# Kernel tuning notes

Hardware: AMD Instinct MI355X
Metric: run time of the kernel (lower is better)

The kernel has to match this reference:

```python
import jax, jax.numpy as jnp
import numpy as np

K = 15  # knn neighbors (init kwarg k)


def setup_inputs() -> dict:
    key = jax.random.key(0)
    ks = jax.random.split(key, 6)
    N, E, IN, H = 4096, 24576, 3, 64
    x = jax.random.normal(ks[0], (N, IN), jnp.float32)
    edges = jax.random.randint(ks[1], (2, E), 0, N, jnp.int32)
    # torch Linear weights: shape [out, in], y = x @ W.T
    Wt = jax.random.normal(ks[2], (H, IN), jnp.float32) * 0.1   # DevConv W_theta
    Wp = jax.random.normal(ks[3], (H, H), jnp.float32) * 0.1    # DevConv W_phi
    Wq = jax.random.normal(ks[4], (H, H), jnp.float32) * 0.1    # W_q
    Wk = jax.random.normal(ks[5], (H, H), jnp.float32) * 0.1    # W_k
    return {"x": x, "edges": edges, "Wt": Wt, "Wp": Wp, "Wq": Wq, "Wk": Wk}


def _knn_edges(x, k):
    # pairwise squared distances via gram trick; exclude self (loop=False)
    N = x.shape[0]
    sq = jnp.sum(x * x, axis=-1)
    d = sq[:, None] + sq[None, :] - 2.0 * (x @ x.T)  # [N, N]
    d = d.at[jnp.arange(N), jnp.arange(N)].set(jnp.inf)
    _, nbr = jax.lax.top_k(-d, k)  # [N, k] nearest neighbor indices
    row = jnp.repeat(jnp.arange(N, dtype=jnp.int32), k)
    col = nbr.reshape(-1).astype(jnp.int32)
    return row, col  # flow='target_to_source': row = center node


def reference(x, edges, Wt, Wp, Wq, Wk):
    N = x.shape[0]
    # ---- knn graph + edge union (dedup is a no-op for max aggregation) ----
    kr, kc = _knn_edges(x, K)
    row_e = jnp.concatenate([edges[0], kr])
    col_e = jnp.concatenate([edges[1], kc])
    # ---- DevConv: f_i = W_phi ( max_{j in N(i)} W_theta (x_j - x_i) ) ----
    diff = x[col_e] - x[row_e]                 # [Etot, IN]
    msg = diff @ Wt.T                          # [Etot, H]
    agg = jax.ops.segment_max(msg, row_e, num_segments=N)
    agg = jnp.where(jnp.isfinite(agg), agg, 0.0)
    feat = agg @ Wp.T                          # [N, H]
    # ---- scatter-softmax attention over original edges ----
    r, c = edges[0], edges[1]
    q = feat @ Wq.T
    k = feat @ Wk.T
    att = jnp.sum(q[r] * k[c], axis=-1)        # [E]
    m = jax.ops.segment_max(att, r, num_segments=N)
    ex = jnp.exp(att - m[r])
    den = jax.ops.segment_sum(ex, r, num_segments=N)
    attn = ex / den[r]
    # ---- estimated adjacency A_s = S @ A @ S^T (dense canonical form) ----
    S = jnp.zeros((N, N), x.dtype).at[r, c].add(attn)   # coalesce = sum dups
    A = jnp.zeros((N, N), x.dtype).at[r, c].add(1.0)
    return (S @ A) @ S.T
```

## Files before the change

kernel.cpp:

```cpp
#include <hip/hip_runtime.h>
#include <math.h>

#define N_NODES 4096
#define H 64
#define NE 24576
#define KNN 15
#define KBUF 448
#define MAXP_ROW 512
#define BSLOT 32

typedef float vfloat4 __attribute__((ext_vector_type(4)));

__device__ __forceinline__ int mbcnt64(unsigned long long m) {
    int lo = __builtin_amdgcn_mbcnt_lo((unsigned int)m, 0u);
    return __builtin_amdgcn_mbcnt_hi((unsigned int)(m >> 32), lo);
}

__global__ __launch_bounds__(256) void k_init(int* __restrict__ cursR, int* __restrict__ cursC,
                                              const float* __restrict__ x, float4* __restrict__ xp,
                                              const float* __restrict__ Wp, const float* __restrict__ Wq,
                                              const float* __restrict__ Wk,
                                              float* __restrict__ WpT, float* __restrict__ WqT,
                                              float* __restrict__ WkT) {
    int tid = blockIdx.x * 256 + threadIdx.x;
    if (tid < N_NODES) {
        cursR[tid] = 0; cursC[tid] = 0;
        float a = x[tid * 3], b = x[tid * 3 + 1], c = x[tid * 3 + 2];
        xp[tid] = make_float4(a, b, c, a * a + b * b + c * c);
    }
    if (tid < H * H) {
        int k = tid >> 6, h = tid & 63;
        WpT[k * H + h] = Wp[h * H + k];
        WqT[k * H + h] = Wq[h * H + k];
        WkT[k * H + h] = Wk[h * H + k];
    }
}

__global__ __launch_bounds__(64) void k_knn(const float4* __restrict__ xp, int* __restrict__ knn_idx,
                                            const int* __restrict__ edges, int* __restrict__ cursR,
                                            int* __restrict__ cursC, int* __restrict__ colRb,
                                            int* __restrict__ c2cb, float2* __restrict__ jav) {
    __shared__ unsigned long long cb[KBUF];
    const int lane = threadIdx.x;
    const int i = blockIdx.x;

    if (i < NE / 64) {
        int e = i * 64 + lane;
        int r = edges[e], c = edges[NE + e];
        int p = atomicAdd(&cursR[r], 1);
        int q = atomicAdd(&cursC[c], 1);
        if (p < BSLOT && q < BSLOT) {
            colRb[r * BSLOT + p] = c;
            c2cb[r * BSLOT + p] = c * BSLOT + q;
            ((int*)jav)[2 * (c * BSLOT + q)] = r;
        }
    }

    const float4 pi = xp[i];
    unsigned long long tauKey;
    int cnt;

    auto sort64 = [&](unsigned long long key) -> unsigned long long {
#pragma unroll
        for (int k = 2; k <= 64; k <<= 1) {
#pragma unroll
            for (int j = 32; j > 0; j >>= 1) {
                if (j >= k) continue;
                unsigned long long other = __shfl_xor(key, j);
                bool asc = ((lane & k) == 0);
                bool takeMin = (((lane & j) == 0) == asc);
                bool less = key < other;
                key = (takeMin == less) ? key : other;
            }
        }
        return key;
    };

    auto tighten = [&]() {
        __builtin_amdgcn_wave_barrier();
        int n = (cnt + 63) >> 6;
        unsigned long long v[7];
        unsigned long long kmin = ~0ull;
#pragma unroll
        for (int t = 0; t < 7; ++t) {
            v[t] = ~0ull;
            if (t < n) {
                int s = t * 64 + lane;
                if (s < cnt) v[t] = cb[s];
                kmin = (v[t] < kmin) ? v[t] : kmin;
            }
        }
        unsigned long long T = __shfl(sort64(kmin), 14);
        __builtin_amdgcn_wave_barrier();
        int m = 0;
#pragma unroll
        for (int t = 0; t < 7; ++t) {
            if (t < n) {
                bool pred = (v[t] <= T);
                unsigned long long mk = __ballot(pred);
                if (pred) cb[m + mbcnt64(mk)] = v[t];
                m += __popcll(mk);
            }
        }
        cnt = m;
        tauKey = T;
        __builtin_amdgcn_wave_barrier();
    };

    {
        unsigned long long kmin = ~0ull;
#pragma unroll
        for (int t = 0; t < 4; ++t) {
            int j = t * 64 + lane;
            float4 pj = xp[j];
            float d = pi.w + pj.w - 2.0f * (pi.x * pj.x + pi.y * pj.y + pi.z * pj.z);
            unsigned long long key = ((unsigned long long)__float_as_uint(d) << 32) | (unsigned)j;
            if (j == i) key = ~0ull;
            cb[j] = key;
            kmin = (key < kmin) ? key : kmin;
        }
        cnt = 256;
        tauKey = __shfl(sort64(kmin), 14);
        __builtin_amdgcn_wave_barrier();
    }

    for (int iter = 1; iter < 16; ++iter) {
        const int jb = iter * 256;
        float4 p0 = xp[jb + lane];
        float4 p1 = xp[jb + 64 + lane];
        float4 p2 = xp[jb + 128 + lane];
        float4 p3 = xp[jb + 192 + lane];
        float d0 = pi.w + p0.w - 2.0f * (pi.x * p0.x + pi.y * p0.y + pi.z * p0.z);
        float d1 = pi.w + p1.w - 2.0f * (pi.x * p1.x + pi.y * p1.y + pi.z * p1.z);
        float d2 = pi.w + p2.w - 2.0f * (pi.x * p2.x + pi.y * p2.y + pi.z * p2.z);
        float d3 = pi.w + p3.w - 2.0f * (pi.x * p3.x + pi.y * p3.y + pi.z * p3.z);
#pragma unroll
        for (int t = 0; t < 4; ++t) {
            float d = (t == 0) ? d0 : (t == 1) ? d1 : (t == 2) ? d2 : d3;
            int j = jb + t * 64 + lane;
            unsigned long long key = ((unsigned long long)__float_as_uint(d) << 32) | (unsigned)j;
            bool pred = (key < tauKey) && (j != i);
            unsigned long long m = __ballot(pred);
            if (m) {
                if (pred) cb[cnt + mbcnt64(m)] = key;
                cnt += __popcll(m);
            }
        }
        if (cnt > KBUF - 256) tighten();
    }

    tighten();
    if (cnt > 64) tighten();
    unsigned long long fin = (lane < cnt) ? cb[lane] : ~0ull;
    fin = sort64(fin);
    if (lane < KNN) knn_idx[i * KNN + lane] = (int)(fin & 0xffffffffu);
}

__global__ __launch_bounds__(256) void k_agg_feat_qk(const float4* __restrict__ xp,
                                                     const int* __restrict__ cursR, const int* __restrict__ colRb,
                                                     const int* __restrict__ knn_idx, const float* __restrict__ Wt,
                                                     const float* __restrict__ WpT, const float* __restrict__ WqT,
                                                     const float* __restrict__ WkT,
                                                     float* __restrict__ qb, float* __restrict__ kb) {
    __shared__ float mrow[4][64];
    __shared__ float frow[4][64];
    int w = threadIdx.x >> 6, lane = threadIdx.x & 63;
    int i = blockIdx.x * 4 + w;
    float w0 = Wt[lane * 3], w1 = Wt[lane * 3 + 1], w2 = Wt[lane * 3 + 2];
    float4 pi = xp[i];
    float m = -INFINITY;
    int deg = cursR[i];
    for (int s = 0; s < deg; ++s) {
        float4 pj = xp[colRb[i * BSLOT + s]];
        m = fmaxf(m, w0 * (pj.x - pi.x) + w1 * (pj.y - pi.y) + w2 * (pj.z - pi.z));
    }
    for (int t = 0; t < KNN; ++t) {
        float4 pj = xp[knn_idx[i * KNN + t]];
        m = fmaxf(m, w0 * (pj.x - pi.x) + w1 * (pj.y - pi.y) + w2 * (pj.z - pi.z));
    }
    if (!(m > -INFINITY)) m = 0.0f;
    mrow[w][lane] = m;
    __syncthreads();
    float f = 0.f;
    for (int k2 = 0; k2 < H; ++k2) f += WpT[k2 * H + lane] * mrow[w][k2];
    frow[w][lane] = f;
    __syncthreads();
    float qv = 0.f, kv = 0.f;
    for (int k2 = 0; k2 < H; ++k2) {
        float fr = frow[w][k2];
        qv += WqT[k2 * H + lane] * fr;
        kv += WkT[k2 * H + lane] * fr;
    }
    qb[i * H + lane] = qv;
    kb[i * H + lane] = kv;
}

__global__ __launch_bounds__(256) void k_attsm(const int* __restrict__ cursR, const int* __restrict__ colRb,
                                               const int* __restrict__ c2cb,
                                               const float* __restrict__ qb, const float* __restrict__ kb,
                                               float* __restrict__ attnRb, float2* __restrict__ jav) {
    int w = threadIdx.x >> 6, lane = threadIdx.x & 63;
    int i = blockIdx.x * 4 + w;
    int deg = cursR[i];
    if (deg == 0) return;
    float qv = qb[i * H + lane];
    float m = -INFINITY, myv = 0.f;
    for (int s = 0; s < deg; ++s) {
        int c = colRb[i * BSLOT + s];
        float v = qv * kb[c * H + lane];
#pragma unroll
        for (int o = 32; o > 0; o >>= 1) v += __shfl_xor(v, o);
        if (lane == s) myv = v;
        m = fmaxf(m, v);
    }
    float ex = (lane < deg) ? expf(myv - m) : 0.f;
    float den = ex;
#pragma unroll
    for (int o = 32; o > 0; o >>= 1) den += __shfl_xor(den, o);
    if (lane < deg) {
        float a = ex / den;
        attnRb[i * BSLOT + lane] = a;
        ((float*)jav)[2 * c2cb[i * BSLOT + lane] + 1] = a;
    }
}

__global__ __launch_bounds__(256) void k_final_row(const int* __restrict__ cursR, const int* __restrict__ cursC,
                                                   const int* __restrict__ colRb, const float* __restrict__ attnRb,
                                                   const float2* __restrict__ jav,
                                                   float* __restrict__ out) {
    __shared__ __align__(16) float Orow[N_NODES];
    __shared__ int   pc2[MAXP_ROW];
    __shared__ float psv[MAXP_ROW];
    __shared__ int npair;
    int r = blockIdx.x;
    int tid = threadIdx.x;
    vfloat4* O4 = (vfloat4*)Orow;
    vfloat4 z = {0.f, 0.f, 0.f, 0.f};

    if (tid >= 64) {
        for (int t = tid - 64; t < N_NODES / 4; t += 192) O4[t] = z;
    } else {
        int lane = tid;
        int base = 0;
        int deg = cursR[r];
        for (int s = 0; s < deg; ++s) {
            int c = colRb[r * BSLOT + s];
            float sv = attnRb[r * BSLOT + s];
            int d = cursR[c];
            for (int a = lane; a < d; a += 64) {
                pc2[base + a] = colRb[c * BSLOT + a];
                psv[base + a] = sv;
            }
            base += d;
        }
        if (lane == 0) npair = base;
    }
    __syncthreads();

    int np = npair;
    for (int p = tid; p < np; p += 256) {
        int c2 = pc2[p];
        float sv = psv[p];
        int b1 = cursC[c2];
        for (int b = 0; b < b1; ++b) {
            float2 v = jav[c2 * BSLOT + b];
            atomicAdd(&Orow[__float_as_int(v.x)], sv * v.y);
        }
    }
    __syncthreads();

    vfloat4* o4 = (vfloat4*)(out + (size_t)r * N_NODES);
#pragma unroll
    for (int t = 0; t < N_NODES / 4 / 256; ++t)
        __builtin_nontemporal_store(O4[tid + t * 256], &o4[tid + t * 256]);
}

extern "C" void kernel_launch(void* const* d_in, const int* in_sizes, int n_in,
                              void* d_out, int out_size, void* d_ws, size_t ws_size,
                              hipStream_t stream) {
    const float* x    = (const float*)d_in[0];
    const int* edges  = (const int*)d_in[1];
    const float* Wt   = (const float*)d_in[2];
    const float* Wp   = (const float*)d_in[3];
    const float* Wq   = (const float*)d_in[4];
    const float* Wk   = (const float*)d_in[5];
    float* out = (float*)d_out;

    char* w = (char*)d_ws;
    size_t off = 0;
    auto alloc = [&](size_t bytes) -> void* {
        void* p = w + off;
        off += (bytes + 255) & ~(size_t)255;
        return p;
    };
    float4* xp      = (float4*)alloc((size_t)N_NODES * 16);
    int*   knn      = (int*)  alloc((size_t)N_NODES * KNN * 4);
    float* qb       = (float*)alloc((size_t)N_NODES * H * 4);
    float* kb       = (float*)alloc((size_t)N_NODES * H * 4);
    int*   cursR    = (int*)  alloc((size_t)N_NODES * 4);
    int*   cursC    = (int*)  alloc((size_t)N_NODES * 4);
    int*   colRb    = (int*)  alloc((size_t)N_NODES * BSLOT * 4);
    int*   c2cb     = (int*)  alloc((size_t)N_NODES * BSLOT * 4);
    float* attnRb   = (float*)alloc((size_t)N_NODES * BSLOT * 4);
    float2* jav     = (float2*)alloc((size_t)N_NODES * BSLOT * 8);
    float* WpT      = (float*)alloc((size_t)H * H * 4);
    float* WqT      = (float*)alloc((size_t)H * H * 4);
    float* WkT      = (float*)alloc((size_t)H * H * 4);

    k_init<<<(N_NODES + 255) / 256, 256, 0, stream>>>(cursR, cursC, x, xp, Wp, Wq, Wk, WpT, WqT, WkT);
    k_knn<<<N_NODES, 64, 0, stream>>>(xp, knn, edges, cursR, cursC, colRb, c2cb, jav);
    k_agg_feat_qk<<<N_NODES / 4, 256, 0, stream>>>(xp, cursR, colRb, knn, Wt, WpT, WqT, WkT, qb, kb);
    k_attsm<<<N_NODES / 4, 256, 0, stream>>>(cursR, colRb, c2cb, qb, kb, attnRb, jav);
    k_final_row<<<N_NODES, 256, 0, stream>>>(cursR, cursC, colRb, attnRb, jav, out);
}
```

Measured before the change: 77.38 us.

## Pack four KNN query nodes per block sharing double-buffered LDS candidate tiles

The KNN kernel now runs four waves per block, each handling one query node. Candidate point tiles are cooperatively loaded into a double-buffered shared-memory stage, with the next tile prefetched into registers. This replaces per-wave redundant global loads of the same points and cuts the block count by four. The cost is two block-wide barriers per iteration, which couple waves whose tighten calls diverge, plus more LDS per block, which may reduce occupancy.

```diff
diff --git a/kernel.cpp b/kernel.cpp
--- a/kernel.cpp
+++ b/kernel.cpp
@@ -36,16 +36,19 @@
     }
 }
 
-__global__ __launch_bounds__(64) void k_knn(const float4* __restrict__ xp, int* __restrict__ knn_idx,
-                                            const int* __restrict__ edges, int* __restrict__ cursR,
-                                            int* __restrict__ cursC, int* __restrict__ colRb,
-                                            int* __restrict__ c2cb, float2* __restrict__ jav) {
-    __shared__ unsigned long long cb[KBUF];
-    const int lane = threadIdx.x;
-    const int i = blockIdx.x;
-
-    if (i < NE / 64) {
-        int e = i * 64 + lane;
+__global__ __launch_bounds__(256) void k_knn(const float4* __restrict__ xp, int* __restrict__ knn_idx,
+                                             const int* __restrict__ edges, int* __restrict__ cursR,
+                                             int* __restrict__ cursC, int* __restrict__ colRb,
+                                             int* __restrict__ c2cb, float2* __restrict__ jav) {
+    __shared__ unsigned long long cb[4][KBUF];
+    __shared__ float4 stage[2][256];
+    const int tid = threadIdx.x;
+    const int w = tid >> 6;
+    const int lane = tid & 63;
+    const int i = blockIdx.x * 4 + w;
+
+    if (blockIdx.x < NE / 256) {
+        int e = blockIdx.x * 256 + tid;
         int r = edges[e], c = edges[NE + e];
         int p = atomicAdd(&cursR[r], 1);
         int q = atomicAdd(&cursC[c], 1);
@@ -86,7 +89,7 @@
             v[t] = ~0ull;
             if (t < n) {
                 int s = t * 64 + lane;
-                if (s < cnt) v[t] = cb[s];
+                if (s < cnt) v[t] = cb[w][s];
                 kmin = (v[t] < kmin) ? v[t] : kmin;
             }
         }
@@ -98,7 +101,7 @@
             if (t < n) {
                 bool pred = (v[t] <= T);
                 unsigned long long mk = __ballot(pred);
-                if (pred) cb[m + mbcnt64(mk)] = v[t];
+                if (pred) cb[w][m + mbcnt64(mk)] = v[t];
                 m += __popcll(mk);
             }
         }
@@ -107,29 +110,38 @@
         __builtin_amdgcn_wave_barrier();
     };
 
+    stage[0][tid] = xp[tid];
+    __syncthreads();
+
     {
+        float4 pf = xp[256 + tid];
         unsigned long long kmin = ~0ull;
 #pragma unroll
         for (int t = 0; t < 4; ++t) {
             int j = t * 64 + lane;
-            float4 pj = xp[j];
+            float4 pj = stage[0][j];
             float d = pi.w + pj.w - 2.0f * (pi.x * pj.x + pi.y * pj.y + pi.z * pj.z);
             unsigned long long key = ((unsigned long long)__float_as_uint(d) << 32) | (unsigned)j;
             if (j == i) key = ~0ull;
-            cb[j] = key;
+            cb[w][j] = key;
             kmin = (key < kmin) ? key : kmin;
         }
         cnt = 256;
         tauKey = __shfl(sort64(kmin), 14);
-        __builtin_amdgcn_wave_barrier();
+        __syncthreads();
+        stage[1][tid] = pf;
+        __syncthreads();
     }
 
     for (int iter = 1; iter < 16; ++iter) {
         const int jb = iter * 256;
-        float4 p0 = xp[jb + lane];
-        float4 p1 = xp[jb + 64 + lane];
-        float4 p2 = xp[jb + 128 + lane];
-        float4 p3 = xp[jb + 192 + lane];
+        const int cur = iter & 1;
+        float4 pf;
+        if (iter < 15) pf = xp[jb + 256 + tid];
+        float4 p0 = stage[cur][lane];
+        float4 p1 = stage[cur][64 + lane];
+        float4 p2 = stage[cur][128 + lane];
+        float4 p3 = stage[cur][192 + lane];
         float d0 = pi.w + p0.w - 2.0f * (pi.x * p0.x + pi.y * p0.y + pi.z * p0.z);
         float d1 = pi.w + p1.w - 2.0f * (pi.x * p1.x + pi.y * p1.y + pi.z * p1.z);
         float d2 = pi.w + p2.w - 2.0f * (pi.x * p2.x + pi.y * p2.y + pi.z * p2.z);
@@ -142,16 +154,21 @@
             bool pred = (key < tauKey) && (j != i);
             unsigned long long m = __ballot(pred);
             if (m) {
-                if (pred) cb[cnt + mbcnt64(m)] = key;
+                if (pred) cb[w][cnt + mbcnt64(m)] = key;
                 cnt += __popcll(m);
             }
         }
         if (cnt > KBUF - 256) tighten();
+        if (iter < 15) {
+            __syncthreads();
+            stage[cur ^ 1][tid] = pf;
+            __syncthreads();
+        }
     }
 
     tighten();
     if (cnt > 64) tighten();
-    unsigned long long fin = (lane < cnt) ? cb[lane] : ~0ull;
+    unsigned long long fin = (lane < cnt) ? cb[w][lane] : ~0ull;
     fin = sort64(fin);
     if (lane < KNN) knn_idx[i * KNN + lane] = (int)(fin & 0xffffffffu);
 }
@@ -308,7 +325,7 @@
     float* WkT      = (float*)alloc((size_t)H * H * 4);
 
     k_init<<<(N_NODES + 255) / 256, 256, 0, stream>>>(cursR, cursC, x, xp, Wp, Wq, Wk, WpT, WqT, WkT);
-    k_knn<<<N_NODES, 64, 0, stream>>>(xp, knn, edges, cursR, cursC, colRb, c2cb, jav);
+    k_knn<<<N_NODES / 4, 256, 0, stream>>>(xp, knn, edges, cursR, cursC, colRb, c2cb, jav);
     k_agg_feat_qk<<<N_NODES / 4, 256, 0, stream>>>(xp, cursR, colRb, knn, Wt, WpT, WqT, WkT, qb, kb);
     k_attsm<<<N_NODES / 4, 256, 0, stream>>>(cursR, colRb, c2cb, qb, kb, attnRb, jav);
     k_final_row<<<N_NODES, 256, 0, stream>>>(cursR, cursC, colRb, attnRb, jav, out);
```

Result: no change. 77.02 us (-0.5%).
